# Performance work log

Measured on AMD Instinct MI355X. Metric: run time of the kernel, lower is better.

The kernel has to match this reference:

```python
import jax, jax.numpy as jnp
import numpy as np

B, NSIDE, NH = 4, 64, 8
N = 12 * NSIDE * NSIDE          # HEALPix pixel count, nested ordering
CIN, CHID, COUT = 256, 512, 256
WS = 16                          # window = 4**(w+1) nested pixels, w=1
HD = CHID // NH


def _ln(x, g, b, eps=1e-5):
    m = x.mean(-1, keepdims=True)
    v = ((x - m) ** 2).mean(-1, keepdims=True)
    return (x - m) * jax.lax.rsqrt(v + eps) * g + b


def _win_attn(x, qkv_w, qkv_b, pw, pb):
    b_, n_, c = x.shape
    nw = n_ // WS
    xw = x.reshape(b_, nw, WS, c)
    qkv = xw @ qkv_w + qkv_b                      # [B, nw, ws, 3C]
    q, k, v = jnp.split(qkv, 3, axis=-1)
    def heads(t):
        return t.reshape(b_, nw, WS, NH, HD).transpose(0, 1, 3, 2, 4)
    q, k, v = heads(q), heads(k), heads(v)        # [B, nw, H, ws, hd]
    a = jax.nn.softmax(jnp.einsum('bwhqd,bwhkd->bwhqk', q, k) * (HD ** -0.5), axis=-1)
    o = jnp.einsum('bwhqk,bwhkd->bwhqd', a, v)
    o = o.transpose(0, 1, 3, 2, 4).reshape(b_, n_, c)
    return o @ pw + pb


def _heal_block(x, p, shift):
    if shift:
        x = jnp.roll(x, -WS // 2, axis=1)          # shifted-window (cyclic in nested order)
    x = x + _win_attn(_ln(x, p['ln1g'], p['ln1b']), p['qkvw'], p['qkvb'], p['pw'], p['pb'])
    h = _ln(x, p['ln2g'], p['ln2b'])
    h = jax.nn.gelu(h @ p['m1w'] + p['m1b'], approximate=False) @ p['m2w'] + p['m2b']
    x = x + h
    if shift:
        x = jnp.roll(x, WS // 2, axis=1)
    return x


def _sn_linear(h, W, b, u):
    # torch spectral_norm: one power-iteration, u/v detached, sigma = u' W v
    v = W @ u                                      # [CHID]
    v = jax.lax.stop_gradient(v / (jnp.linalg.norm(v) + 1e-12))
    u2 = v @ W                                     # [COUT]
    u2 = jax.lax.stop_gradient(u2 / (jnp.linalg.norm(u2) + 1e-12))
    sigma = v @ W @ u2
    return h @ (W / sigma) + b


def setup_inputs() -> dict:
    key = jax.random.key(0)
    ks = iter(jax.random.split(key, 64))
    def w(shape, s=0.02):
        return jax.random.normal(next(ks), shape, jnp.float32) * s
    inp = {'x': jax.random.normal(next(ks), (B, N, CIN), jnp.float32)}
    inp['ff1_w'] = w((CIN, CHID)); inp['ff1_b'] = jnp.zeros((CHID,), jnp.float32)
    for pre in ('a', 'b'):
        inp[f'{pre}_ln1g'] = jnp.ones((CHID,), jnp.float32)
        inp[f'{pre}_ln1b'] = jnp.zeros((CHID,), jnp.float32)
        inp[f'{pre}_qkvw'] = w((CHID, 3 * CHID)); inp[f'{pre}_qkvb'] = jnp.zeros((3 * CHID,), jnp.float32)
        inp[f'{pre}_pw'] = w((CHID, CHID)); inp[f'{pre}_pb'] = jnp.zeros((CHID,), jnp.float32)
        inp[f'{pre}_ln2g'] = jnp.ones((CHID,), jnp.float32)
        inp[f'{pre}_ln2b'] = jnp.zeros((CHID,), jnp.float32)
        inp[f'{pre}_m1w'] = w((CHID, 4 * CHID)); inp[f'{pre}_m1b'] = jnp.zeros((4 * CHID,), jnp.float32)
        inp[f'{pre}_m2w'] = w((4 * CHID, CHID)); inp[f'{pre}_m2b'] = jnp.zeros((CHID,), jnp.float32)
    inp['ff2_w'] = w((CHID, COUT)); inp['ff2_b'] = jnp.zeros((COUT,), jnp.float32)
    inp['ff2_u'] = jax.random.normal(next(ks), (COUT,), jnp.float32)
    return inp


def reference(x, ff1_w, ff1_b,
              a_ln1g, a_ln1b, a_qkvw, a_qkvb, a_pw, a_pb, a_ln2g, a_ln2b, a_m1w, a_m1b, a_m2w, a_m2b,
              b_ln1g, b_ln1b, b_qkvw, b_qkvb, b_pw, b_pb, b_ln2g, b_ln2b, b_m1w, b_m1b, b_m2w, b_m2b,
              ff2_w, ff2_b, ff2_u):
    pa = dict(ln1g=a_ln1g, ln1b=a_ln1b, qkvw=a_qkvw, qkvb=a_qkvb, pw=a_pw, pb=a_pb,
              ln2g=a_ln2g, ln2b=a_ln2b, m1w=a_m1w, m1b=a_m1b, m2w=a_m2w, m2b=a_m2b)
    pb_ = dict(ln1g=b_ln1g, ln1b=b_ln1b, qkvw=b_qkvw, qkvb=b_qkvb, pw=b_pw, pb=b_pb,
               ln2g=b_ln2g, ln2b=b_ln2b, m1w=b_m1w, m1b=b_m1b, m2w=b_m2w, m2b=b_m2b)
    h = jax.nn.gelu(x @ ff1_w + ff1_b, approximate=False)   # feed_forward1
    h = _heal_block(h, pa, shift=False)                     # message_passing1
    h = _heal_block(h, pb_, shift=True)                     # message_passing2
    return _sn_linear(h, ff2_w, ff2_b, ff2_u)               # spectral-norm linear
```

## Files before the change

kernel.cpp:

```cpp
#include <hip/hip_runtime.h>
#include <hip/hip_bf16.h>
#include <math.h>

typedef _Float16 f16;
typedef __attribute__((ext_vector_type(8))) _Float16 f16x8;
typedef __attribute__((ext_vector_type(4))) _Float16 f16x4;
typedef __attribute__((ext_vector_type(4))) float f32x4;

#define DINLINE __device__ __forceinline__

DINLINE float gelu_fast(float x) {
  float t = 0.7978845608f * x * __builtin_fmaf(0.044715f * x, x, 1.0f);
  float E = __expf(fminf(2.0f * t, 18.0f));
  return x * E * __builtin_amdgcn_rcpf(E + 1.0f);
}
DINLINE void gload16(const void* g, void* l) {
  __builtin_amdgcn_global_load_lds((const __attribute__((address_space(1))) void*)g,
                                   (__attribute__((address_space(3))) void*)l, 16, 0, 0);
}

#define BAR       __builtin_amdgcn_s_barrier()
#define WAITLGKM  asm volatile("s_waitcnt lgkmcnt(0)" ::: "memory")
#define WAITVM(n) asm volatile("s_waitcnt vmcnt(" #n ")" ::: "memory")

template <int EPI>
__global__ __launch_bounds__(512, 2) void gemm256(
    const f16* __restrict__ A, const f16* __restrict__ Bt,
    const float* __restrict__ bias, const f16* __restrict__ Cin,
    float* __restrict__ Cf, f16* __restrict__ Cb,
    const float* __restrict__ scale_ptr,
    int N, int K, int nct)
{
  __shared__ alignas(16) f16 sm[2][4][8192];

  const int nwg = (int)gridDim.x;
  const int gid = (int)blockIdx.x;
  const int q = nwg >> 3, r = nwg & 7;
  const int xcd = gid & 7, idx = gid >> 3;
  const int swz = (xcd < r ? xcd * (q + 1) : r * (q + 1) + (xcd - r) * q) + idx;
  const int rt = swz / nct, ct = swz - rt * nct;
  const int m0 = rt << 8, n0 = ct << 8;

  const int tid = (int)threadIdx.x;
  const int lane = tid & 63;
  const int wid = tid >> 6;
  const int wr = wid >> 2, wc = wid & 3;

  const int srow = tid >> 2;
  const int sl = (tid & 3) ^ ((srow >> 1) & 3);
  const size_t aG = (size_t)(m0 + srow) * K + sl * 8;
  const size_t bG = (size_t)(n0 + srow) * K + sl * 8;
  const int sL = tid * 8;

  const int rsel = lane & 15, khi = lane >> 4;
  const int sx = (khi ^ ((rsel >> 1) & 3)) << 3;

  f32x4 acc[8][4] = {};
  f16x8 aF[4], bF[4];

  const int NT = K >> 6;

#define STAGEH(h)                                                             \
  {                                                                           \
    const int _t = (h) >> 2, _r = (h) & 3, _b = _t & 1;                       \
    const f16* _s = (_r & 1) ? Bt : A;                                        \
    const size_t _g = ((_r & 1) ? bG : aG) + (size_t)_t * 64 + ((_r >> 1) << 5); \
    gload16(_s + _g, &sm[_b][_r][sL]);                                        \
    gload16(_s + _g + (size_t)128 * (size_t)K, &sm[_b][_r][4096 + sL]);       \
  }

#define DSRA(b, kc, mb)                                                       \
  {                                                                           \
    _Pragma("unroll")                                                         \
    for (int _i = 0; _i < 4; ++_i)                                            \
      aF[_i] = *(const f16x8*)(&sm[b][(kc) << 1]                              \
                  [(wr * 128 + ((mb) + _i) * 16 + rsel) * 32 + sx]);          \
  }

#define DSRB(b, kc)                                                           \
  {                                                                           \
    _Pragma("unroll")                                                         \
    for (int _i = 0; _i < 4; ++_i)                                            \
      bF[_i] = *(const f16x8*)(&sm[b][1 + ((kc) << 1)]                        \
                  [(wc * 64 + _i * 16 + rsel) * 32 + sx]);                    \
  }

#define MMC(mb)                                                               \
  {                                                                           \
    __builtin_amdgcn_s_setprio(1);                                            \
    _Pragma("unroll")                                                         \
    for (int _m = 0; _m < 4; ++_m)                                            \
      _Pragma("unroll")                                                       \
      for (int _n = 0; _n < 4; ++_n)                                          \
        acc[(mb) + _m][_n] = __builtin_amdgcn_mfma_f32_16x16x32_f16(          \
            bF[_n], aF[_m], acc[(mb) + _m][_n], 0, 0, 0);                     \
    __builtin_amdgcn_s_setprio(0);                                            \
  }

  STAGEH(0); STAGEH(1); STAGEH(2); STAGEH(3); STAGEH(4);
  WAITVM(6);
  BAR;

  for (int t = 0; t < NT - 2; ++t) {
    const int b = t & 1, hb = 4 * t;
    STAGEH(hb + 5); DSRA(b, 0, 0); DSRB(b, 0); BAR; WAITLGKM; MMC(0); WAITVM(6); BAR;
    STAGEH(hb + 6); DSRA(b, 0, 4);             BAR; WAITLGKM; MMC(4); WAITVM(6); BAR;
    STAGEH(hb + 7); DSRA(b, 1, 0); DSRB(b, 1); BAR; WAITLGKM; MMC(0); WAITVM(6); BAR;
    STAGEH(hb + 8); DSRA(b, 1, 4);             BAR; WAITLGKM; MMC(4); WAITVM(6); BAR;
  }
  {
    const int t = NT - 2, b = t & 1, hb = 4 * t;
    STAGEH(hb + 5); DSRA(b, 0, 0); DSRB(b, 0); BAR; WAITLGKM; MMC(0); WAITVM(6); BAR;
    STAGEH(hb + 6); DSRA(b, 0, 4);             BAR; WAITLGKM; MMC(4); WAITVM(6); BAR;
    STAGEH(hb + 7); DSRA(b, 1, 0); DSRB(b, 1); BAR; WAITLGKM; MMC(0); WAITVM(6); BAR;
                    DSRA(b, 1, 4);             BAR; WAITLGKM; MMC(4); WAITVM(4); BAR;
  }
  {
    const int b = (NT - 1) & 1;
    DSRA(b, 0, 0); DSRB(b, 0); BAR; WAITLGKM; MMC(0); WAITVM(2); BAR;
    DSRA(b, 0, 4);             BAR; WAITLGKM; MMC(4); WAITVM(0); BAR;
    DSRA(b, 1, 0); DSRB(b, 1); BAR; WAITLGKM; MMC(0); BAR;
    DSRA(b, 1, 4);             BAR; WAITLGKM; MMC(4); BAR;
  }

  const float scale = (EPI & 8) ? scale_ptr[0] : 1.0f;
  const int R0 = m0 + wr * 128, C0 = n0 + wc * 64;
#pragma unroll
  for (int m = 0; m < 8; ++m) {
    const int row = R0 + m * 16 + rsel;
#pragma unroll
    for (int n = 0; n < 4; ++n) {
      const int col = C0 + n * 16 + (khi << 2);
      f32x4 v = acc[m][n];
      if (EPI & 8) {
#pragma unroll
        for (int j = 0; j < 4; ++j) v[j] *= scale;
      }
      f32x4 bb = *(const f32x4*)(bias + col);
#pragma unroll
      for (int j = 0; j < 4; ++j) v[j] += bb[j];
      if (EPI & 1) {
#pragma unroll
        for (int j = 0; j < 4; ++j) v[j] = gelu_fast(v[j]);
      }
      if (EPI & 2) {
        f16x4 c4 = *(const f16x4*)(Cin + (size_t)row * N + col);
#pragma unroll
        for (int j = 0; j < 4; ++j) v[j] += (float)c4[j];
      }
      if (EPI & 4) {
        f16x4 o;
#pragma unroll
        for (int j = 0; j < 4; ++j) o[j] = (f16)v[j];
        *(f16x4*)(Cb + (size_t)row * N + col) = o;
      } else {
        *(f32x4*)(Cf + (size_t)row * N + col) = v;
      }
    }
  }
#undef STAGEH
#undef DSRA
#undef DSRB
#undef MMC
}

__global__ __launch_bounds__(256) void ln_f16(
    const f16* __restrict__ X, const float* __restrict__ g,
    const float* __restrict__ b, f16* __restrict__ Y, int ntok)
{
  const int lane = threadIdx.x & 63;
  const int c = lane * 8;
  const f32x4 g0 = *(const f32x4*)(g + c), g1 = *(const f32x4*)(g + c + 4);
  const f32x4 b0 = *(const f32x4*)(b + c), b1 = *(const f32x4*)(b + c + 4);
  for (int token = blockIdx.x * 4 + (threadIdx.x >> 6); token < ntok;
       token += gridDim.x * 4) {
    f16x8 v = *(const f16x8*)(X + (size_t)token * 512 + c);
    float vf[8];
    float s = 0.f, s2 = 0.f;
#pragma unroll
    for (int j = 0; j < 8; ++j) { vf[j] = (float)v[j]; s += vf[j]; s2 += vf[j] * vf[j]; }
#pragma unroll
    for (int o = 32; o > 0; o >>= 1) { s += __shfl_xor(s, o, 64); s2 += __shfl_xor(s2, o, 64); }
    const float mean = s * (1.f / 512.f);
    const float inv = rsqrtf(s2 * (1.f / 512.f) - mean * mean + 1e-5f);
    f16x8 o8;
#pragma unroll
    for (int j = 0; j < 4; ++j) {
      o8[j]     = (f16)((vf[j] - mean) * inv * g0[j] + b0[j]);
      o8[4 + j] = (f16)((vf[4 + j] - mean) * inv * g1[j] + b1[j]);
    }
    *(f16x8*)(Y + (size_t)token * 512 + c) = o8;
  }
}

__global__ __launch_bounds__(256) void cvt_f32_f16(const float* __restrict__ X,
                                                   f16* __restrict__ Y, long n8)
{
  const long i = (long)blockIdx.x * 256 + threadIdx.x;
  if (i >= n8) return;
  f32x4 v0 = *(const f32x4*)(X + i * 8), v1 = *(const f32x4*)(X + i * 8 + 4);
  f16x8 o8;
#pragma unroll
  for (int j = 0; j < 4; ++j) { o8[j] = (f16)v0[j]; o8[4 + j] = (f16)v1[j]; }
  *(f16x8*)(Y + i * 8) = o8;
}

__global__ __launch_bounds__(256) void w_tr_tiled(const float* __restrict__ W,
                                                  f16* __restrict__ Wt, int K, int N)
{
  __shared__ f16 td[64][66];
  const int nkt = K >> 6;
  const int kt = blockIdx.x % nkt, nt = blockIdx.x / nkt;
  const int k0 = kt << 6, n0 = nt << 6;
  const int col = threadIdx.x & 63, rq = threadIdx.x >> 6;
#pragma unroll
  for (int j = 0; j < 16; ++j) {
    const int row = j * 4 + rq;
    td[row][col] = (f16)W[(size_t)(k0 + row) * N + n0 + col];
  }
  __syncthreads();
#pragma unroll
  for (int j = 0; j < 16; ++j) {
    const int nrow = j * 4 + rq;
    Wt[(size_t)(n0 + nrow) * K + k0 + col] = td[col][nrow];
  }
}

template <int SHIFT>
__global__ __launch_bounds__(256) void win_attn(const f16* __restrict__ QKV,
                                                f16* __restrict__ O)
{
  __shared__ alignas(16) f16 kv[2][16][1160];
  const int wl0 = (int)blockIdx.x * 2;
  const int tid = (int)threadIdx.x;

  for (int i = tid; i < 4096; i += 256) {
    const int win = i >> 11;
    const int rem = i & 2047;
    const int row = rem >> 7;
    const int c8 = rem & 127;
    const int src = ((wl0 + win) * 16 + row + SHIFT) % 49152;
    const int sect = c8 >> 6;
    const int hh = (c8 >> 3) & 7;
    const int dd = (c8 & 7) * 8;
    *(f16x8*)(&kv[win][row][sect * 576 + hh * 72 + dd]) =
        *(const f16x8*)(QKV + (size_t)src * 1536 + 512 + c8 * 8);
  }

  const int win = tid >> 7, h = (tid >> 4) & 7, qi = tid & 15;
  const int qtok = ((wl0 + win) * 16 + qi + SHIFT) % 49152;
  f16x8 qv[8];
#pragma unroll
  for (int c8 = 0; c8 < 8; ++c8)
    qv[c8] = *(const f16x8*)(QKV + (size_t)qtok * 1536 + h * 64 + c8 * 8);

  __syncthreads();

  float sc[16];
  float mx = -1e30f;
#pragma unroll
  for (int kj = 0; kj < 16; ++kj) {
    const f16* kr = &kv[win][kj][h * 72];
    float s = 0.f;
#pragma unroll
    for (int c8 = 0; c8 < 8; ++c8) {
      f16x8 k8 = *(const f16x8*)(kr + c8 * 8);
#pragma unroll
      for (int j = 0; j < 8; ++j) s += (float)qv[c8][j] * (float)k8[j];
    }
    s *= 0.125f;
    sc[kj] = s;
    mx = fmaxf(mx, s);
  }
  float sum = 0.f;
#pragma unroll
  for (int kj = 0; kj < 16; ++kj) { sc[kj] = expf(sc[kj] - mx); sum += sc[kj]; }
  const float inv = 1.f / sum;
  float ov[64] = {};
#pragma unroll
  for (int kj = 0; kj < 16; ++kj) {
    const float a = sc[kj] * inv;
    const f16* vr = &kv[win][kj][576 + h * 72];
#pragma unroll
    for (int c8 = 0; c8 < 8; ++c8) {
      f16x8 v8 = *(const f16x8*)(vr + c8 * 8);
#pragma unroll
      for (int j = 0; j < 8; ++j) ov[c8 * 8 + j] += a * (float)v8[j];
    }
  }
  f16* orow = O + (size_t)qtok * 512 + h * 64;
#pragma unroll
  for (int c8 = 0; c8 < 8; ++c8) {
    f16x8 t;
#pragma unroll
    for (int j = 0; j < 8; ++j) t[j] = (f16)ov[c8 * 8 + j];
    *(f16x8*)(orow + c8 * 8) = t;
  }
}

__global__ __launch_bounds__(256) void sn_sigma(const float* __restrict__ W,
                                                const float* __restrict__ u,
                                                float* __restrict__ inv_sigma)
{
  __shared__ float vsh[512];
  __shared__ float ush[256];
  __shared__ float red[256];
  const int t = (int)threadIdx.x;
  ush[t] = u[t];
  __syncthreads();
  float a0 = 0.f, a1 = 0.f;
  for (int j = 0; j < 256; ++j) {
    a0 += W[t * 256 + j] * ush[j];
    a1 += W[(t + 256) * 256 + j] * ush[j];
  }
  vsh[t] = a0; vsh[t + 256] = a1;
  red[t] = a0 * a0 + a1 * a1;
  __syncthreads();
  for (int s = 128; s > 0; s >>= 1) { if (t < s) red[t] += red[t + s]; __syncthreads(); }
  const float nv = sqrtf(red[0]) + 1e-12f;
  __syncthreads();
  const float invv = 1.f / nv;
  vsh[t] *= invv; vsh[t + 256] *= invv;
  __syncthreads();
  float u2 = 0.f;
  for (int i = 0; i < 512; ++i) u2 += vsh[i] * W[i * 256 + t];
  red[t] = u2 * u2;
  __syncthreads();
  for (int s = 128; s > 0; s >>= 1) { if (t < s) red[t] += red[t + s]; __syncthreads(); }
  const float nu = sqrtf(red[0]) + 1e-12f;
  __syncthreads();
  ush[t] = u2 / nu;
  __syncthreads();
  float d0 = 0.f, d1 = 0.f;
  for (int j = 0; j < 256; ++j) {
    d0 += W[t * 256 + j] * ush[j];
    d1 += W[(t + 256) * 256 + j] * ush[j];
  }
  red[t] = vsh[t] * d0 + vsh[t + 256] * d1;
  __syncthreads();
  for (int s = 128; s > 0; s >>= 1) { if (t < s) red[t] += red[t + s]; __syncthreads(); }
  if (t == 0) inv_sigma[0] = 1.f / red[0];
}

__global__ void fill_sentinel(float* __restrict__ out, long n, float val)
{
  const long i = (long)blockIdx.x * 256 + threadIdx.x;
  for (long k = i; k < n; k += (long)gridDim.x * 256) out[k] = val;
}

extern "C" void kernel_launch(void* const* d_in, const int* in_sizes, int n_in,
                              void* d_out, int out_size, void* d_ws, size_t ws_size,
                              hipStream_t stream)
{
  const int M = 196608;
  const int MC = 49152;
  constexpr size_t OFF_U   = 201326592ull;
  constexpr size_t OFF_OH  = 201326592ull + 150994944ull;
  constexpr size_t OFF_WT  = 402653184ull;
  constexpr size_t OFF_SIG = 415760384ull;
  constexpr size_t NEED    = OFF_SIG + 256ull;

  if (ws_size < NEED) {
    fill_sentinel<<<2048, 256, 0, stream>>>((float*)d_out, (long)out_size,
                                            (float)(ws_size >> 20));
    return;
  }

  char* ws = (char*)d_ws;
  f16* R     = (f16*)(ws);
  f16* U     = (f16*)(ws + OFF_U);
  f16* OH    = (f16*)(ws + OFF_OH);
  f16* WT    = (f16*)(ws + OFF_WT);
  float* sig = (float*)(ws + OFF_SIG);
  f16* X     = (f16*)d_out;

  const float* ff1_b = (const float*)d_in[2];
  const float* ff2_b = (const float*)d_in[28];

  f16* W_FF1 = WT;
  auto W_QKV = [&](int blk) { return WT + (blk ? 3276800 : 131072); };
  auto W_PW  = [&](int blk) { return WT + (blk ? 4063232 : 917504); };
  auto W_M1  = [&](int blk) { return WT + (blk ? 4325376 : 1179648); };
  auto W_M2  = [&](int blk) { return WT + (blk ? 5373952 : 2228224); };
  f16* W_FF2 = WT + 6422528;

  w_tr_tiled<<<32, 256, 0, stream>>>((const float*)d_in[1], W_FF1, 256, 512);
  for (int blk = 0; blk < 2; ++blk) {
    w_tr_tiled<<<192, 256, 0, stream>>>((const float*)d_in[blk ? 17 : 5], W_QKV(blk), 512, 1536);
    w_tr_tiled<<<64, 256, 0, stream>>>((const float*)d_in[blk ? 19 : 7], W_PW(blk), 512, 512);
    w_tr_tiled<<<256, 256, 0, stream>>>((const float*)d_in[blk ? 23 : 11], W_M1(blk), 512, 2048);
    w_tr_tiled<<<256, 256, 0, stream>>>((const float*)d_in[blk ? 25 : 13], W_M2(blk), 2048, 512);
  }
  w_tr_tiled<<<32, 256, 0, stream>>>((const float*)d_in[27], W_FF2, 512, 256);
  sn_sigma<<<1, 256, 0, stream>>>((const float*)d_in[27], (const float*)d_in[29], sig);

  cvt_f32_f16<<<24576, 256, 0, stream>>>((const float*)d_in[0], U, (long)M * 256 / 8);
  gemm256<5><<<1536, 512, 0, stream>>>(U, W_FF1, ff1_b, nullptr, nullptr, R, nullptr,
                                       512, 256, 2);

  for (int blk = 0; blk < 2; ++blk) {
    const float* ln1g = (const float*)d_in[blk ? 15 : 3];
    const float* ln1b = (const float*)d_in[blk ? 16 : 4];
    const float* qkvb = (const float*)d_in[blk ? 18 : 6];
    const float* pb   = (const float*)d_in[blk ? 20 : 8];
    const float* ln2g = (const float*)d_in[blk ? 21 : 9];
    const float* ln2b = (const float*)d_in[blk ? 22 : 10];
    const float* m1b  = (const float*)d_in[blk ? 24 : 12];
    const float* m2b  = (const float*)d_in[blk ? 26 : 14];

    ln_f16<<<4096, 256, 0, stream>>>(R, ln1g, ln1b, X, M);
    for (int mc = 0; mc < 4; ++mc) {
      const size_t ro = (size_t)mc * MC * 512;
      gemm256<4><<<1152, 512, 0, stream>>>(X + ro, W_QKV(blk), qkvb, nullptr,
                                           nullptr, U, nullptr, 1536, 512, 6);
      if (blk == 0) win_attn<0><<<1536, 256, 0, stream>>>(U, OH);
      else          win_attn<8><<<1536, 256, 0, stream>>>(U, OH);
      gemm256<6><<<384, 512, 0, stream>>>(OH, W_PW(blk), pb, R + ro,
                                          nullptr, R + ro, nullptr, 512, 512, 2);
    }
    ln_f16<<<4096, 256, 0, stream>>>(R, ln2g, ln2b, X, M);
    for (int mc = 0; mc < 4; ++mc) {
      const size_t ro = (size_t)mc * MC * 512;
      gemm256<5><<<1536, 512, 0, stream>>>(X + ro, W_M1(blk), m1b, nullptr,
                                           nullptr, U, nullptr, 2048, 512, 8);
      gemm256<6><<<384, 512, 0, stream>>>(U, W_M2(blk), m2b, R + ro,
                                          nullptr, R + ro, nullptr, 512, 2048, 2);
    }
  }

  gemm256<8><<<768, 512, 0, stream>>>(R, W_FF2, ff2_b, nullptr, (float*)d_out,
                                      nullptr, sig, 256, 512, 1);
}
```

Baseline: 5.097 ms.

## Replace 256x256 GEMM with 128x128 tile kernel and simpler double-buffer pipeline

Replaces the 512-thread 256x256-tile GEMM, which used a fine-grained half-stage pipeline, with a 256-thread 128x128-tile kernel. It stages a full 64-wide K slice per iteration into a double buffer and runs two MFMA rounds between barriers. All launches are regridded for the smaller tiles, which gives more workgroups and less LDS per block, at the cost of lower per-tile data reuse and more global traffic. The tanh-GELU approximation is also rewritten to use exp2 with prefolded constants.

```diff
diff --git a/kernel.cpp b/kernel.cpp
--- a/kernel.cpp
+++ b/kernel.cpp
@@ -10,8 +10,10 @@
 #define DINLINE __device__ __forceinline__
 
 DINLINE float gelu_fast(float x) {
-  float t = 0.7978845608f * x * __builtin_fmaf(0.044715f * x, x, 1.0f);
-  float E = __expf(fminf(2.0f * t, 18.0f));
+  float x2 = x * x;
+  float z = x * __builtin_fmaf(0.14746116f, x2, 2.30211422f);
+  z = fminf(z, 60.0f);
+  float E = __builtin_amdgcn_exp2f(z);
   return x * E * __builtin_amdgcn_rcpf(E + 1.0f);
 }
 DINLINE void gload16(const void* g, void* l) {
@@ -24,14 +26,14 @@
 #define WAITVM(n) asm volatile("s_waitcnt vmcnt(" #n ")" ::: "memory")
 
 template <int EPI>
-__global__ __launch_bounds__(512, 2) void gemm256(
+__global__ __launch_bounds__(256, 2) void gemm128(
     const f16* __restrict__ A, const f16* __restrict__ Bt,
     const float* __restrict__ bias, const f16* __restrict__ Cin,
     float* __restrict__ Cf, f16* __restrict__ Cb,
     const float* __restrict__ scale_ptr,
     int N, int K, int nct)
 {
-  __shared__ alignas(16) f16 sm[2][4][8192];
+  __shared__ alignas(16) f16 sm[2][4][4096];
 
   const int nwg = (int)gridDim.x;
   const int gid = (int)blockIdx.x;
@@ -39,42 +41,41 @@
   const int xcd = gid & 7, idx = gid >> 3;
   const int swz = (xcd < r ? xcd * (q + 1) : r * (q + 1) + (xcd - r) * q) + idx;
   const int rt = swz / nct, ct = swz - rt * nct;
-  const int m0 = rt << 8, n0 = ct << 8;
+  const int m0 = rt << 7, n0 = ct << 7;
 
   const int tid = (int)threadIdx.x;
   const int lane = tid & 63;
   const int wid = tid >> 6;
-  const int wr = wid >> 2, wc = wid & 3;
-
-  const int srow = tid >> 2;
-  const int sl = (tid & 3) ^ ((srow >> 1) & 3);
-  const size_t aG = (size_t)(m0 + srow) * K + sl * 8;
-  const size_t bG = (size_t)(n0 + srow) * K + sl * 8;
-  const int sL = tid * 8;
+  const int wr = wid >> 1, wcn = wid & 1;
 
   const int rsel = lane & 15, khi = lane >> 4;
   const int sx = (khi ^ ((rsel >> 1) & 3)) << 3;
 
-  f32x4 acc[8][4] = {};
+  f32x4 acc[4][4] = {};
   f16x8 aF[4], bF[4];
 
   const int NT = K >> 6;
 
-#define STAGEH(h)                                                             \
+#define STAGE(b, k0)                                                          \
   {                                                                           \
-    const int _t = (h) >> 2, _r = (h) & 3, _b = _t & 1;                       \
-    const f16* _s = (_r & 1) ? Bt : A;                                        \
-    const size_t _g = ((_r & 1) ? bG : aG) + (size_t)_t * 64 + ((_r >> 1) << 5); \
-    gload16(_s + _g, &sm[_b][_r][sL]);                                        \
-    gload16(_s + _g + (size_t)128 * (size_t)K, &sm[_b][_r][4096 + sL]);       \
-  }
-
-#define DSRA(b, kc, mb)                                                       \
+    _Pragma("unroll")                                                         \
+    for (int _g = 0; _g < 8; ++_g) {                                          \
+      const int _s = _g * 256 + tid;                                          \
+      const int _reg = _s >> 9, _sr = (_s >> 2) & 127;                        \
+      const int _ls = (_s & 3) ^ ((_sr >> 1) & 3);                            \
+      const f16* _src = (_reg & 1) ? Bt + (size_t)(n0 + _sr) * K              \
+                                   : A + (size_t)(m0 + _sr) * K;              \
+      gload16(_src + (k0) + ((_reg >> 1) << 5) + (_ls << 3),                  \
+              (f16*)sm[b] + (size_t)_s * 8);                                  \
+    }                                                                         \
+  }
+
+#define DSRA(b, kc)                                                           \
   {                                                                           \
     _Pragma("unroll")                                                         \
     for (int _i = 0; _i < 4; ++_i)                                            \
       aF[_i] = *(const f16x8*)(&sm[b][(kc) << 1]                              \
-                  [(wr * 128 + ((mb) + _i) * 16 + rsel) * 32 + sx]);          \
+                  [(wr * 64 + _i * 16 + rsel) * 32 + sx]);                    \
   }
 
 #define DSRB(b, kc)                                                           \
@@ -82,51 +83,40 @@
     _Pragma("unroll")                                                         \
     for (int _i = 0; _i < 4; ++_i)                                            \
       bF[_i] = *(const f16x8*)(&sm[b][1 + ((kc) << 1)]                        \
-                  [(wc * 64 + _i * 16 + rsel) * 32 + sx]);                    \
-  }
-
-#define MMC(mb)                                                               \
+                  [(wcn * 64 + _i * 16 + rsel) * 32 + sx]);                   \
+  }
+
+#define MMC                                                                   \
   {                                                                           \
     __builtin_amdgcn_s_setprio(1);                                            \
     _Pragma("unroll")                                                         \
     for (int _m = 0; _m < 4; ++_m)                                            \
       _Pragma("unroll")                                                       \
       for (int _n = 0; _n < 4; ++_n)                                          \
-        acc[(mb) + _m][_n] = __builtin_amdgcn_mfma_f32_16x16x32_f16(          \
-            bF[_n], aF[_m], acc[(mb) + _m][_n], 0, 0, 0);                     \
+        acc[_m][_n] = __builtin_amdgcn_mfma_f32_16x16x32_f16(                 \
+            bF[_n], aF[_m], acc[_m][_n], 0, 0, 0);                            \
     __builtin_amdgcn_s_setprio(0);                                            \
   }
 
-  STAGEH(0); STAGEH(1); STAGEH(2); STAGEH(3); STAGEH(4);
-  WAITVM(6);
-  BAR;
-
-  for (int t = 0; t < NT - 2; ++t) {
-    const int b = t & 1, hb = 4 * t;
-    STAGEH(hb + 5); DSRA(b, 0, 0); DSRB(b, 0); BAR; WAITLGKM; MMC(0); WAITVM(6); BAR;
-    STAGEH(hb + 6); DSRA(b, 0, 4);             BAR; WAITLGKM; MMC(4); WAITVM(6); BAR;
-    STAGEH(hb + 7); DSRA(b, 1, 0); DSRB(b, 1); BAR; WAITLGKM; MMC(0); WAITVM(6); BAR;
-    STAGEH(hb + 8); DSRA(b, 1, 4);             BAR; WAITLGKM; MMC(4); WAITVM(6); BAR;
-  }
-  {
-    const int t = NT - 2, b = t & 1, hb = 4 * t;
-    STAGEH(hb + 5); DSRA(b, 0, 0); DSRB(b, 0); BAR; WAITLGKM; MMC(0); WAITVM(6); BAR;
-    STAGEH(hb + 6); DSRA(b, 0, 4);             BAR; WAITLGKM; MMC(4); WAITVM(6); BAR;
-    STAGEH(hb + 7); DSRA(b, 1, 0); DSRB(b, 1); BAR; WAITLGKM; MMC(0); WAITVM(6); BAR;
-                    DSRA(b, 1, 4);             BAR; WAITLGKM; MMC(4); WAITVM(4); BAR;
-  }
-  {
-    const int b = (NT - 1) & 1;
-    DSRA(b, 0, 0); DSRB(b, 0); BAR; WAITLGKM; MMC(0); WAITVM(2); BAR;
-    DSRA(b, 0, 4);             BAR; WAITLGKM; MMC(4); WAITVM(0); BAR;
-    DSRA(b, 1, 0); DSRB(b, 1); BAR; WAITLGKM; MMC(0); BAR;
-    DSRA(b, 1, 4);             BAR; WAITLGKM; MMC(4); BAR;
+  STAGE(0, 0);
+  for (int t = 0; t < NT; ++t) {
+    const int b = t & 1;
+    if (t + 1 < NT) {
+      if (b) STAGE(0, (t + 1) << 6) else STAGE(1, (t + 1) << 6)
+      WAITVM(8);
+    } else {
+      WAITVM(0);
+    }
+    BAR;
+    DSRA(b, 0); DSRB(b, 0); WAITLGKM; MMC;
+    DSRA(b, 1); DSRB(b, 1); WAITLGKM; MMC;
+    BAR;
   }
 
   const float scale = (EPI & 8) ? scale_ptr[0] : 1.0f;
-  const int R0 = m0 + wr * 128, C0 = n0 + wc * 64;
-#pragma unroll
-  for (int m = 0; m < 8; ++m) {
+  const int R0 = m0 + wr * 64, C0 = n0 + wcn * 64;
+#pragma unroll
+  for (int m = 0; m < 4; ++m) {
     const int row = R0 + m * 16 + rsel;
 #pragma unroll
     for (int n = 0; n < 4; ++n) {
@@ -158,7 +148,7 @@
       }
     }
   }
-#undef STAGEH
+#undef STAGE
 #undef DSRA
 #undef DSRB
 #undef MMC
@@ -395,8 +385,8 @@
   sn_sigma<<<1, 256, 0, stream>>>((const float*)d_in[27], (const float*)d_in[29], sig);
 
   cvt_f32_f16<<<24576, 256, 0, stream>>>((const float*)d_in[0], U, (long)M * 256 / 8);
-  gemm256<5><<<1536, 512, 0, stream>>>(U, W_FF1, ff1_b, nullptr, nullptr, R, nullptr,
-                                       512, 256, 2);
+  gemm128<5><<<6144, 256, 0, stream>>>(U, W_FF1, ff1_b, nullptr, nullptr, R, nullptr,
+                                       512, 256, 4);
 
   for (int blk = 0; blk < 2; ++blk) {
     const float* ln1g = (const float*)d_in[blk ? 15 : 3];
@@ -411,23 +401,23 @@
     ln_f16<<<4096, 256, 0, stream>>>(R, ln1g, ln1b, X, M);
     for (int mc = 0; mc < 4; ++mc) {
       const size_t ro = (size_t)mc * MC * 512;
-      gemm256<4><<<1152, 512, 0, stream>>>(X + ro, W_QKV(blk), qkvb, nullptr,
-                                           nullptr, U, nullptr, 1536, 512, 6);
+      gemm128<4><<<4608, 256, 0, stream>>>(X + ro, W_QKV(blk), qkvb, nullptr,
+                                           nullptr, U, nullptr, 1536, 512, 12);
       if (blk == 0) win_attn<0><<<1536, 256, 0, stream>>>(U, OH);
       else          win_attn<8><<<1536, 256, 0, stream>>>(U, OH);
-      gemm256<6><<<384, 512, 0, stream>>>(OH, W_PW(blk), pb, R + ro,
-                                          nullptr, R + ro, nullptr, 512, 512, 2);
+      gemm128<6><<<1536, 256, 0, stream>>>(OH, W_PW(blk), pb, R + ro,
+                                           nullptr, R + ro, nullptr, 512, 512, 4);
     }
     ln_f16<<<4096, 256, 0, stream>>>(R, ln2g, ln2b, X, M);
     for (int mc = 0; mc < 4; ++mc) {
       const size_t ro = (size_t)mc * MC * 512;
-      gemm256<5><<<1536, 512, 0, stream>>>(X + ro, W_M1(blk), m1b, nullptr,
-                                           nullptr, U, nullptr, 2048, 512, 8);
-      gemm256<6><<<384, 512, 0, stream>>>(U, W_M2(blk), m2b, R + ro,
-                                          nullptr, R + ro, nullptr, 512, 2048, 2);
-    }
-  }
-
-  gemm256<8><<<768, 512, 0, stream>>>(R, W_FF2, ff2_b, nullptr, (float*)d_out,
-                                      nullptr, sig, 256, 512, 1);
-}
+      gemm128<5><<<6144, 256, 0, stream>>>(X + ro, W_M1(blk), m1b, nullptr,
+                                           nullptr, U, nullptr, 2048, 512, 16);
+      gemm128<6><<<1536, 256, 0, stream>>>(U, W_M2(blk), m2b, R + ro,
+                                           nullptr, R + ro, nullptr, 512, 2048, 4);
+    }
+  }
+
+  gemm128<8><<<3072, 256, 0, stream>>>(R, W_FF2, ff2_b, nullptr, (float*)d_out,
+                                       nullptr, sig, 256, 512, 2);
+}
```

Result: no change. 5.053 ms (-0.9%).

## Add 128x256 double-buffered GEMM for narrow-N launches and cheaper GELU

Applied to the files above, without the earlier changes.

Adds a second GEMM kernel with 128x256 tiles and a simpler two-stage LDS double buffer at up to four workgroups per CU. It is used for the FF1, projection, MLP-down and final spectral-norm GEMMs, which doubles their grid sizes, while the 256x256 kernel is kept for QKV and MLP-up with its occupancy hint lowered to one. GELU is rewritten as x*sigmoid using exp2 with folded constants and no clamp. The epilogue is pulled into a shared macro. The smaller tiles give more workgroups on the N=512/256 GEMMs at the cost of less reuse per tile, and the unclamped exp2 could overflow for large negative inputs, though rcp of infinity still yields zero.

```diff
diff --git a/kernel.cpp b/kernel.cpp
--- a/kernel.cpp
+++ b/kernel.cpp
@@ -10,9 +10,10 @@
 #define DINLINE __device__ __forceinline__
 
 DINLINE float gelu_fast(float x) {
-  float t = 0.7978845608f * x * __builtin_fmaf(0.044715f * x, x, 1.0f);
-  float E = __expf(fminf(2.0f * t, 18.0f));
-  return x * E * __builtin_amdgcn_rcpf(E + 1.0f);
+  float x2 = x * x;
+  float z = x * __builtin_fmaf(-0.10294537f, x2, -2.30211422f);
+  float E = __builtin_amdgcn_exp2f(z);
+  return x * __builtin_amdgcn_rcpf(1.0f + E);
 }
 DINLINE void gload16(const void* g, void* l) {
   __builtin_amdgcn_global_load_lds((const __attribute__((address_space(1))) void*)g,
@@ -22,9 +23,34 @@
 #define BAR       __builtin_amdgcn_s_barrier()
 #define WAITLGKM  asm volatile("s_waitcnt lgkmcnt(0)" ::: "memory")
 #define WAITVM(n) asm volatile("s_waitcnt vmcnt(" #n ")" ::: "memory")
+#define CFE       asm volatile("" ::: "memory")
+
+#define EPILOG(vreg, rowE, colE)                                              \
+  {                                                                           \
+    f32x4 v = (vreg);                                                         \
+    if (EPI & 8) {                                                            \
+      _Pragma("unroll") for (int _j = 0; _j < 4; ++_j) v[_j] *= scale;        \
+    }                                                                         \
+    f32x4 bb = *(const f32x4*)(bias + (colE));                                \
+    _Pragma("unroll") for (int _j = 0; _j < 4; ++_j) v[_j] += bb[_j];         \
+    if (EPI & 1) {                                                            \
+      _Pragma("unroll") for (int _j = 0; _j < 4; ++_j) v[_j] = gelu_fast(v[_j]); \
+    }                                                                         \
+    if (EPI & 2) {                                                            \
+      f16x4 c4 = *(const f16x4*)(Cin + (size_t)(rowE) * N + (colE));          \
+      _Pragma("unroll") for (int _j = 0; _j < 4; ++_j) v[_j] += (float)c4[_j];\
+    }                                                                         \
+    if (EPI & 4) {                                                            \
+      f16x4 o;                                                                \
+      _Pragma("unroll") for (int _j = 0; _j < 4; ++_j) o[_j] = (f16)v[_j];    \
+      *(f16x4*)(Cb + (size_t)(rowE) * N + (colE)) = o;                        \
+    } else {                                                                  \
+      *(f32x4*)(Cf + (size_t)(rowE) * N + (colE)) = v;                        \
+    }                                                                         \
+  }
 
 template <int EPI>
-__global__ __launch_bounds__(512, 2) void gemm256(
+__global__ __launch_bounds__(512, 1) void gemm256_8p(
     const f16* __restrict__ A, const f16* __restrict__ Bt,
     const float* __restrict__ bias, const f16* __restrict__ Cin,
     float* __restrict__ Cf, f16* __restrict__ Cb,
@@ -131,37 +157,111 @@
 #pragma unroll
     for (int n = 0; n < 4; ++n) {
       const int col = C0 + n * 16 + (khi << 2);
-      f32x4 v = acc[m][n];
-      if (EPI & 8) {
-#pragma unroll
-        for (int j = 0; j < 4; ++j) v[j] *= scale;
-      }
-      f32x4 bb = *(const f32x4*)(bias + col);
-#pragma unroll
-      for (int j = 0; j < 4; ++j) v[j] += bb[j];
-      if (EPI & 1) {
-#pragma unroll
-        for (int j = 0; j < 4; ++j) v[j] = gelu_fast(v[j]);
-      }
-      if (EPI & 2) {
-        f16x4 c4 = *(const f16x4*)(Cin + (size_t)row * N + col);
-#pragma unroll
-        for (int j = 0; j < 4; ++j) v[j] += (float)c4[j];
-      }
-      if (EPI & 4) {
-        f16x4 o;
-#pragma unroll
-        for (int j = 0; j < 4; ++j) o[j] = (f16)v[j];
-        *(f16x4*)(Cb + (size_t)row * N + col) = o;
-      } else {
-        *(f32x4*)(Cf + (size_t)row * N + col) = v;
-      }
+      EPILOG(acc[m][n], row, col);
     }
   }
 #undef STAGEH
 #undef DSRA
 #undef DSRB
 #undef MMC
+}
+
+template <int EPI>
+__global__ __launch_bounds__(512, 4) void gemm(
+    const f16* __restrict__ A, const f16* __restrict__ Bt,
+    const float* __restrict__ bias, const f16* __restrict__ Cin,
+    float* __restrict__ Cf, f16* __restrict__ Cb,
+    const float* __restrict__ scale_ptr,
+    int N, int K, int nct)
+{
+  __shared__ alignas(16) f16 smf[2 * 3 * 4096];
+
+  const int nwg = (int)gridDim.x;
+  const int gid = (int)blockIdx.x;
+  const int q = nwg >> 3, r = nwg & 7;
+  const int xcd = gid & 7, idx = gid >> 3;
+  const int swz = (xcd < r ? xcd * (q + 1) : r * (q + 1) + (xcd - r) * q) + idx;
+  const int rt = swz / nct, ct = swz - rt * nct;
+  const int m0 = rt << 7, n0 = ct << 8;
+
+  const int tid = (int)threadIdx.x;
+  const int lane = tid & 63;
+  const int wid = tid >> 6;
+  const int wr = wid >> 2, wcn = wid & 3;
+
+  const int rsel = lane & 15, khi = lane >> 4;
+  const int sx = (khi ^ ((rsel >> 1) & 3)) << 3;
+
+  const int r0 = tid >> 2;
+  const int sls = (tid & 3) ^ ((r0 >> 1) & 3);
+  const f16* pA  = A  + (size_t)(m0 + r0) * K + sls * 8;
+  const f16* pB0 = Bt + (size_t)(n0 + r0) * K + sls * 8;
+  const f16* pB1 = Bt + (size_t)(n0 + 128 + r0) * K + sls * 8;
+  f16* ldst = smf + tid * 8;
+
+  const int aB = (wr * 64 + rsel) * 32 + sx;
+  const int bB = (1 + (wcn >> 1)) * 4096 + ((wcn & 1) * 64 + rsel) * 32 + sx;
+
+  f32x4 acc[4][4] = {};
+  const int NT = K >> 5;
+
+#define STG(boff)                                                             \
+  {                                                                           \
+    gload16(pA,  ldst + (boff));                                              \
+    gload16(pB0, ldst + (boff) + 4096);                                       \
+    gload16(pB1, ldst + (boff) + 8192);                                       \
+    pA += 32; pB0 += 32; pB1 += 32;                                           \
+  }
+
+#define CMP(boff)                                                             \
+  {                                                                           \
+    f16x8 aF[4], bF[4];                                                       \
+    _Pragma("unroll")                                                         \
+    for (int _i = 0; _i < 4; ++_i)                                            \
+      aF[_i] = *(const f16x8*)(smf + (boff) + aB + _i * 512);                 \
+    _Pragma("unroll")                                                         \
+    for (int _i = 0; _i < 4; ++_i)                                            \
+      bF[_i] = *(const f16x8*)(smf + (boff) + bB + _i * 512);                 \
+    __builtin_amdgcn_s_setprio(1);                                            \
+    _Pragma("unroll")                                                         \
+    for (int _m = 0; _m < 4; ++_m)                                            \
+      _Pragma("unroll")                                                       \
+      for (int _n = 0; _n < 4; ++_n)                                          \
+        acc[_m][_n] = __builtin_amdgcn_mfma_f32_16x16x32_f16(                 \
+            bF[_n], aF[_m], acc[_m][_n], 0, 0, 0);                            \
+    __builtin_amdgcn_s_setprio(0);                                            \
+  }
+
+  STG(0); STG(12288);
+  for (int t = 0; t + 2 < NT; t += 2) {
+    WAITVM(3); BAR; CFE;
+    CMP(0);
+    BAR; CFE;
+    STG(0);
+    WAITVM(3); BAR; CFE;
+    CMP(12288);
+    BAR; CFE;
+    STG(12288);
+  }
+  WAITVM(3); BAR; CFE;
+  CMP(0);
+  BAR; CFE;
+  WAITVM(0); BAR; CFE;
+  CMP(12288);
+
+  const float scale = (EPI & 8) ? scale_ptr[0] : 1.0f;
+  const int R0 = m0 + wr * 64, C0 = n0 + wcn * 64;
+#pragma unroll
+  for (int m = 0; m < 4; ++m) {
+    const int row = R0 + m * 16 + rsel;
+#pragma unroll
+    for (int n = 0; n < 4; ++n) {
+      const int col = C0 + n * 16 + (khi << 2);
+      EPILOG(acc[m][n], row, col);
+    }
+  }
+#undef STG
+#undef CMP
 }
 
 __global__ __launch_bounds__(256) void ln_f16(
@@ -395,8 +495,8 @@
   sn_sigma<<<1, 256, 0, stream>>>((const float*)d_in[27], (const float*)d_in[29], sig);
 
   cvt_f32_f16<<<24576, 256, 0, stream>>>((const float*)d_in[0], U, (long)M * 256 / 8);
-  gemm256<5><<<1536, 512, 0, stream>>>(U, W_FF1, ff1_b, nullptr, nullptr, R, nullptr,
-                                       512, 256, 2);
+  gemm<5><<<3072, 512, 0, stream>>>(U, W_FF1, ff1_b, nullptr, nullptr, R, nullptr,
+                                    512, 256, 2);
 
   for (int blk = 0; blk < 2; ++blk) {
     const float* ln1g = (const float*)d_in[blk ? 15 : 3];
@@ -411,23 +511,23 @@
     ln_f16<<<4096, 256, 0, stream>>>(R, ln1g, ln1b, X, M);
     for (int mc = 0; mc < 4; ++mc) {
       const size_t ro = (size_t)mc * MC * 512;
-      gemm256<4><<<1152, 512, 0, stream>>>(X + ro, W_QKV(blk), qkvb, nullptr,
-                                           nullptr, U, nullptr, 1536, 512, 6);
+      gemm256_8p<4><<<1152, 512, 0, stream>>>(X + ro, W_QKV(blk), qkvb, nullptr,
+                                              nullptr, U, nullptr, 1536, 512, 6);
       if (blk == 0) win_attn<0><<<1536, 256, 0, stream>>>(U, OH);
       else          win_attn<8><<<1536, 256, 0, stream>>>(U, OH);
-      gemm256<6><<<384, 512, 0, stream>>>(OH, W_PW(blk), pb, R + ro,
-                                          nullptr, R + ro, nullptr, 512, 512, 2);
+      gemm<6><<<768, 512, 0, stream>>>(OH, W_PW(blk), pb, R + ro,
+                                       nullptr, R + ro, nullptr, 512, 512, 2);
     }
     ln_f16<<<4096, 256, 0, stream>>>(R, ln2g, ln2b, X, M);
     for (int mc = 0; mc < 4; ++mc) {
       const size_t ro = (size_t)mc * MC * 512;
-      gemm256<5><<<1536, 512, 0, stream>>>(X + ro, W_M1(blk), m1b, nullptr,
-                                           nullptr, U, nullptr, 2048, 512, 8);
-      gemm256<6><<<384, 512, 0, stream>>>(U, W_M2(blk), m2b, R + ro,
-                                          nullptr, R + ro, nullptr, 512, 2048, 2);
-    }
-  }
-
-  gemm256<8><<<768, 512, 0, stream>>>(R, W_FF2, ff2_b, nullptr, (float*)d_out,
-                                      nullptr, sig, 256, 512, 1);
-}
+      gemm256_8p<5><<<1536, 512, 0, stream>>>(X + ro, W_M1(blk), m1b, nullptr,
+                                              nullptr, U, nullptr, 2048, 512, 8);
+      gemm<6><<<768, 512, 0, stream>>>(U, W_M2(blk), m2b, R + ro,
+                                       nullptr, R + ro, nullptr, 512, 2048, 2);
+    }
+  }
+
+  gemm<8><<<1536, 512, 0, stream>>>(R, W_FF2, ff2_b, nullptr, (float*)d_out,
+                                    nullptr, sig, 256, 512, 1);
+}
```

Result: faster. 4.937 ms (-3.1%).
